# Kernel optimization log

Measured on AMD Instinct MI355X. Metric: run time of the kernel, lower is better.

The kernel has to match this reference:

```python
import jax, jax.numpy as jnp
import numpy as np

N, C = 1024, 256
LN_EPS = 1e-5

def mish(x):
    return x * jnp.tanh(jax.nn.softplus(x))

def layer_norm(x, g, b):
    mu = jnp.mean(x, axis=-1, keepdims=True)
    var = jnp.var(x, axis=-1, keepdims=True)
    return (x - mu) * jax.lax.rsqrt(var + LN_EPS) * g + b

def setup_inputs() -> dict:
    key = jax.random.key(0)
    ks = jax.random.split(key, 8)
    s = 1.0 / np.sqrt(C)
    f32 = jnp.float32
    return {
        "feat": jax.random.normal(ks[0], (N, C), f32),
        # linear_q: Linear(C,C,bias) + LayerNorm + Mish
        "Wq": jax.random.normal(ks[1], (C, C), f32) * s,
        "bq": jnp.zeros((C,), f32),
        "gq": jnp.ones((C,), f32),
        "betaq": jnp.zeros((C,), f32),
        # linear_k
        "Wk": jax.random.normal(ks[2], (C, C), f32) * s,
        "bk": jnp.zeros((C,), f32),
        "gk": jnp.ones((C,), f32),
        "betak": jnp.zeros((C,), f32),
        # linear_v (plain Linear)
        "Wv": jax.random.normal(ks[3], (C, C), f32) * s,
        "bv": jnp.zeros((C,), f32),
        # weight_encoding: Linear + LN + Mish + Linear
        "W1": jax.random.normal(ks[4], (C, C), f32) * s,
        "b1": jnp.zeros((C,), f32),
        "g1": jnp.ones((C,), f32),
        "beta1": jnp.zeros((C,), f32),
        "W2": jax.random.normal(ks[5], (C, C), f32) * s,
        "b2": jnp.zeros((C,), f32),
    }

def reference(feat, Wq, bq, gq, betaq, Wk, bk, gk, betak, Wv, bv,
              W1, b1, g1, beta1, W2, b2):
    # q, k: Linear -> LayerNorm -> Mish ; v: Linear
    q = mish(layer_norm(feat @ Wq + bq, gq, betaq))        # [N, C]
    k = mish(layer_norm(feat @ Wk + bk, gk, betak))        # [N, C]
    v = feat @ Wv + bv                                     # [N, C]
    # relation_qk[i, j, c] = k[i, c] - q[i, j]  (key.unsqueeze(-2) - query.unsqueeze(-1))
    rel = k[:, None, :] - q[:, :, None]                    # [N, C, C]
    # weight_encoding over last axis
    h = mish(layer_norm(rel @ W1 + b1, g1, beta1)) @ W2 + b2  # [N, C, C]
    w = jax.nn.softmax(h, axis=-2)                         # softmax over dim j
    # einsum('ijk,ik->ik'): out[i,k] = (sum_j w[i,j,k]) * v[i,k]
    out = jnp.einsum('ijk,ik->ik', w, v)                   # [N, C]
    return out
```

## Files before the change

kernel.cpp:

```cpp
#include <hip/hip_runtime.h>


#define NN 1024
#define CC 256
#define TM 4

__global__ __launch_bounds__(256) void v_bias_gemm(
    const float* __restrict__ feat,
    const float* __restrict__ Wv,
    const float* __restrict__ bv,
    float* __restrict__ out)
{
    const int c = threadIdx.x;
    const int row0 = blockIdx.x * TM;
    const float* __restrict__ f0 = feat + row0 * CC;

    const float b = bv[c];
    float acc0 = b, acc1 = b, acc2 = b, acc3 = b;

    #pragma unroll 8
    for (int k = 0; k < CC; ++k) {
        const float w = Wv[k * CC + c];
        acc0 = fmaf(f0[0 * CC + k], w, acc0);
        acc1 = fmaf(f0[1 * CC + k], w, acc1);
        acc2 = fmaf(f0[2 * CC + k], w, acc2);
        acc3 = fmaf(f0[3 * CC + k], w, acc3);
    }

    out[(row0 + 0) * CC + c] = acc0;
    out[(row0 + 1) * CC + c] = acc1;
    out[(row0 + 2) * CC + c] = acc2;
    out[(row0 + 3) * CC + c] = acc3;
}

extern "C" void kernel_launch(void* const* d_in, const int* in_sizes, int n_in,
                              void* d_out, int out_size, void* d_ws, size_t ws_size,
                              hipStream_t stream) {
    (void)in_sizes; (void)n_in; (void)d_ws; (void)ws_size; (void)out_size;
    const float* feat = (const float*)d_in[0];
    const float* Wv   = (const float*)d_in[9];
    const float* bv   = (const float*)d_in[10];
    float* out = (float*)d_out;

    dim3 grid(NN / TM);
    dim3 block(CC);
    v_bias_gemm<<<grid, block, 0, stream>>>(feat, Wv, bv, out);
}
```

Baseline: 96.15 us.

## Split the K dimension 16 ways with float4 columns and an LDS reduction

The v-projection GEMM now splits the 256-long K loop across 16 wavefronts per block, each covering 16 k values. Each lane computes four adjacent output columns using float4 weight loads. Partial sums go to a 64KB shared array and are then reduced, with the bias added during the reduction. This shortens each thread's serial FMA chain and raises the number of threads per block, at the cost of extra LDS traffic, a block-wide barrier and high LDS use per block that may limit occupancy.

```diff
diff --git a/kernel.cpp b/kernel.cpp
--- a/kernel.cpp
+++ b/kernel.cpp
@@ -4,33 +4,58 @@
 #define NN 1024
 #define CC 256
 #define TM 4
+#define KS 16
+#define KL (CC / KS)
 
-__global__ __launch_bounds__(256) void v_bias_gemm(
+__global__ __launch_bounds__(1024, 4) void v_bias_gemm_splitk16(
     const float* __restrict__ feat,
     const float* __restrict__ Wv,
     const float* __restrict__ bv,
     float* __restrict__ out)
 {
-    const int c = threadIdx.x;
+    __shared__ float red[KS][TM][CC];
+
+    const int tid  = threadIdx.x;
+    const int lane = tid & 63;
+    const int c4   = lane * 4;
+    const int ks   = __builtin_amdgcn_readfirstlane(tid >> 6);
     const int row0 = blockIdx.x * TM;
-    const float* __restrict__ f0 = feat + row0 * CC;
 
-    const float b = bv[c];
-    float acc0 = b, acc1 = b, acc2 = b, acc3 = b;
+    const float* __restrict__ f0 = feat + row0 * CC + ks * KL;
+    const float* __restrict__ wv = Wv + (ks * KL) * CC + c4;
 
-    #pragma unroll 8
-    for (int k = 0; k < CC; ++k) {
-        const float w = Wv[k * CC + c];
-        acc0 = fmaf(f0[0 * CC + k], w, acc0);
-        acc1 = fmaf(f0[1 * CC + k], w, acc1);
-        acc2 = fmaf(f0[2 * CC + k], w, acc2);
-        acc3 = fmaf(f0[3 * CC + k], w, acc3);
+    float4 a0 = {0.f, 0.f, 0.f, 0.f};
+    float4 a1 = a0, a2 = a0, a3 = a0;
+
+    #pragma unroll
+    for (int k = 0; k < KL; ++k) {
+        const float4 w = *(const float4*)(wv + k * CC);
+        const float s0 = f0[0 * CC + k];
+        const float s1 = f0[1 * CC + k];
+        const float s2 = f0[2 * CC + k];
+        const float s3 = f0[3 * CC + k];
+        a0.x = fmaf(s0, w.x, a0.x); a0.y = fmaf(s0, w.y, a0.y);
+        a0.z = fmaf(s0, w.z, a0.z); a0.w = fmaf(s0, w.w, a0.w);
+        a1.x = fmaf(s1, w.x, a1.x); a1.y = fmaf(s1, w.y, a1.y);
+        a1.z = fmaf(s1, w.z, a1.z); a1.w = fmaf(s1, w.w, a1.w);
+        a2.x = fmaf(s2, w.x, a2.x); a2.y = fmaf(s2, w.y, a2.y);
+        a2.z = fmaf(s2, w.z, a2.z); a2.w = fmaf(s2, w.w, a2.w);
+        a3.x = fmaf(s3, w.x, a3.x); a3.y = fmaf(s3, w.y, a3.y);
+        a3.z = fmaf(s3, w.z, a3.z); a3.w = fmaf(s3, w.w, a3.w);
     }
 
-    out[(row0 + 0) * CC + c] = acc0;
-    out[(row0 + 1) * CC + c] = acc1;
-    out[(row0 + 2) * CC + c] = acc2;
-    out[(row0 + 3) * CC + c] = acc3;
+    *(float4*)&red[ks][0][c4] = a0;
+    *(float4*)&red[ks][1][c4] = a1;
+    *(float4*)&red[ks][2][c4] = a2;
+    *(float4*)&red[ks][3][c4] = a3;
+    __syncthreads();
+
+    const int r = tid >> 8;
+    const int c = tid & (CC - 1);
+    float s = red[0][r][c];
+    #pragma unroll
+    for (int ss = 1; ss < KS; ++ss) s += red[ss][r][c];
+    out[(row0 + r) * CC + c] = s + bv[c];
 }
 
 extern "C" void kernel_launch(void* const* d_in, const int* in_sizes, int n_in,
@@ -43,6 +68,6 @@
     float* out = (float*)d_out;
 
     dim3 grid(NN / TM);
-    dim3 block(CC);
-    v_bias_gemm<<<grid, block, 0, stream>>>(feat, Wv, bv, out);
+    dim3 block(KS * 64);
+    v_bias_gemm_splitk16<<<grid, block, 0, stream>>>(feat, Wv, bv, out);
 }
```

Result: faster. 85.39 us (-11.2%).
